# Optimization experiments

Measured on AMD Instinct MI355X. Metric: run time of the kernel, lower is better.

Reference implementation:

```python
import jax, jax.numpy as jnp
import numpy as np

B, N, D, P = 64, 1024, 256, 256


def setup_inputs() -> dict:
    key = jax.random.key(0)
    kx, k1, k2, k4 = jax.random.split(key, 4)
    x = jax.random.normal(kx, (B, N, D), dtype=jnp.float32)
    # weights ~ random_uniform(-0.05, 0.05) in the original; scale here is irrelevant for math
    w1 = jax.random.uniform(k1, (D, P), dtype=jnp.float32, minval=-0.05, maxval=0.05)
    w2 = jax.random.uniform(k2, (D, P), dtype=jnp.float32, minval=-0.05, maxval=0.05)
    w4 = jax.random.uniform(k4, (P, 1), dtype=jnp.float32, minval=-0.05, maxval=0.05)
    return {"x": x, "w1": w1, "w2": w2, "w4": w4}


def reference(x, w1, w2, w4):
    # x: [B, N, D] (already stacked/transposed; query_n=key_n=values=x in the original)
    q = jax.nn.sigmoid(jnp.einsum('bnd,dp->bnp', x, w1))  # [B,N,P]
    k = jax.nn.sigmoid(jnp.einsum('bnd,dp->bnp', x, w2))  # [B,N,P]
    temper = jnp.sqrt(jnp.asarray(w1.shape[1], x.dtype))
    attn = jax.nn.softmax(jnp.einsum('bnp,bmp->bnm', q, k) / temper, axis=2)  # [B,N,N]
    # dropout(0.1) in the original is inference-identity here
    out = jnp.einsum('bnm,bmd->bnd', attn, x)             # [B,N,D]
    a = jax.nn.softmax(jnp.einsum('bnd,do->bno', out, w4), axis=1)  # [B,N,1]
    sentence = jnp.sum(x * a, axis=1)                     # [B,D]
    return sentence
```

## Files before the change

kernel.cpp:

```cpp
#include <hip/hip_runtime.h>
#include <hip/hip_bf16.h>
#include <cstdint>
#include <cstddef>

constexpr int BB = 64;
constexpr int NN = 1024;
constexpr int DD = 256;
constexpr int PP = 256;

typedef short short8 __attribute__((ext_vector_type(8)));
typedef float f32x4 __attribute__((ext_vector_type(4)));

__device__ __forceinline__ unsigned short f2bf(float f) {
    union { __hip_bfloat16 h; unsigned short u; } v;
    v.h = __float2bfloat16(f);
    return v.u;
}

__device__ __forceinline__ void async_load16(void* lds, const void* g) {
    __builtin_amdgcn_global_load_lds(
        (const __attribute__((address_space(1))) unsigned int*)g,
        (__attribute__((address_space(3))) unsigned int*)lds, 16, 0, 0);
}

__device__ __forceinline__ void stage_tile(const unsigned short* src_base,
                                           unsigned short* lds, int wv, int lane) {
    const char* base = (const char*)src_base;
    char* dst0 = (char*)lds + wv * 8192;
    #pragma unroll
    for (int i = 0; i < 8; i++) {
        int row = wv * 16 + i * 2 + (lane >> 5);
        int blk = (lane & 31) ^ (row & 7);
        async_load16(dst0 + i * 1024, base + row * 512 + blk * 16);
    }
}

__device__ __forceinline__ void stage32(const unsigned short* base,
                                        unsigned short* lds, int wv, int lane) {
    char* dst0 = (char*)lds + wv * 4096;
    #pragma unroll
    for (int i = 0; i < 4; i++) {
        int row = wv * 8 + i * 2 + (lane >> 5);
        int blk = (lane & 31) ^ (row & 7);
        async_load16(dst0 + i * 1024, (const char*)base + row * 512 + blk * 16);
    }
}

__device__ __forceinline__ short8 lds_frag(const unsigned short* lds, int row, int kidx) {
    uint32_t byte = (uint32_t)(row * 512) + (uint32_t)(((kidx ^ (row & 7)) & 31) << 4);
    return *reinterpret_cast<const short8*>(reinterpret_cast<const char*>(lds) + byte);
}

__global__ void prep_wt(const float* __restrict__ w1, const float* __restrict__ w2,
                        unsigned short* __restrict__ wt) {
    int j = blockIdx.x;
    int d = threadIdx.x;
    const float* w = (j < PP) ? w1 : w2;
    int jj = j & (PP - 1);
    wt[j * DD + d] = f2bf(w[d * PP + jj]);
}

__global__ __launch_bounds__(256) void qk_fused(const float* __restrict__ x,
                                                const unsigned short* __restrict__ wt,
                                                const float* __restrict__ w4,
                                                unsigned short* __restrict__ qb,
                                                unsigned short* __restrict__ kb,
                                                float* __restrict__ xv) {
    __shared__ __align__(16) unsigned short wtile[2][16384];
    const int t = threadIdx.x, wv = t >> 6, lane = t & 63, l15 = lane & 15, l4 = lane >> 4;
    const int rowBase = blockIdx.x * 128 + wv * 32;

    stage_tile(wt, wtile[0], wv, lane);

    short8 xf[2][8];
    float xvp[2] = {0.f, 0.f};
    #pragma unroll
    for (int kc = 0; kc < 8; kc++) {
        float4 w4a = *reinterpret_cast<const float4*>(w4 + kc * 32 + l4 * 8);
        float4 w4b = *reinterpret_cast<const float4*>(w4 + kc * 32 + l4 * 8 + 4);
        #pragma unroll
        for (int s = 0; s < 2; s++) {
            const float* xr = x + (size_t)(rowBase + s * 16 + l15) * DD + kc * 32 + l4 * 8;
            float4 a = *reinterpret_cast<const float4*>(xr);
            float4 b = *reinterpret_cast<const float4*>(xr + 4);
            xvp[s] += a.x * w4a.x + a.y * w4a.y + a.z * w4a.z + a.w * w4a.w
                    + b.x * w4b.x + b.y * w4b.y + b.z * w4b.z + b.w * w4b.w;
            short8 f;
            f[0] = (short)f2bf(a.x); f[1] = (short)f2bf(a.y);
            f[2] = (short)f2bf(a.z); f[3] = (short)f2bf(a.w);
            f[4] = (short)f2bf(b.x); f[5] = (short)f2bf(b.y);
            f[6] = (short)f2bf(b.z); f[7] = (short)f2bf(b.w);
            xf[s][kc] = f;
        }
    }
    #pragma unroll
    for (int s = 0; s < 2; s++) {
        xvp[s] += __shfl_xor(xvp[s], 16);
        xvp[s] += __shfl_xor(xvp[s], 32);
        if (l4 == 0) xv[rowBase + s * 16 + l15] = xvp[s];
    }

    __syncthreads();
    int buf = 0;
    for (int ct = 0; ct < 8; ct++) {
        if (ct + 1 < 8) stage_tile(wt + (size_t)(ct + 1) * 64 * DD, wtile[buf ^ 1], wv, lane);
        unsigned short* outp = (ct < 4) ? qb : kb;
        const int pc0 = (ct & 3) * 64;
        #pragma unroll
        for (int st = 0; st < 4; st++) {
            f32x4 acc0 = {0.f, 0.f, 0.f, 0.f};
            f32x4 acc1 = {0.f, 0.f, 0.f, 0.f};
            #pragma unroll
            for (int kc = 0; kc < 8; kc++) {
                short8 wf = lds_frag(wtile[buf], st * 16 + l15, kc * 4 + l4);
                acc0 = __builtin_amdgcn_mfma_f32_16x16x32_bf16(wf, xf[0][kc], acc0, 0, 0, 0);
                acc1 = __builtin_amdgcn_mfma_f32_16x16x32_bf16(wf, xf[1][kc], acc1, 0, 0, 0);
            }
            const int pc = pc0 + st * 16 + l4 * 4;
            ushort4 pk;
            pk.x = f2bf(1.f / (1.f + __expf(-acc0[0])));
            pk.y = f2bf(1.f / (1.f + __expf(-acc0[1])));
            pk.z = f2bf(1.f / (1.f + __expf(-acc0[2])));
            pk.w = f2bf(1.f / (1.f + __expf(-acc0[3])));
            *reinterpret_cast<ushort4*>(outp + (size_t)(rowBase + l15) * PP + pc) = pk;
            pk.x = f2bf(1.f / (1.f + __expf(-acc1[0])));
            pk.y = f2bf(1.f / (1.f + __expf(-acc1[1])));
            pk.z = f2bf(1.f / (1.f + __expf(-acc1[2])));
            pk.w = f2bf(1.f / (1.f + __expf(-acc1[3])));
            *reinterpret_cast<ushort4*>(outp + (size_t)(rowBase + 16 + l15) * PP + pc) = pk;
        }
        __syncthreads();
        buf ^= 1;
    }
}

__global__ __launch_bounds__(256, 2) void attn_logit(const unsigned short* __restrict__ qb,
                                                     const unsigned short* __restrict__ kb,
                                                     const float* __restrict__ xv,
                                                     float* __restrict__ numo,
                                                     float* __restrict__ deno) {
    __shared__ __align__(16) unsigned short kt[2][8192];
    __shared__ float xvs[512];
    const int qt = blockIdx.x >> 1, half = blockIdx.x & 1, b = blockIdx.y;
    const int t = threadIdx.x, wv = t >> 6, lane = t & 63, l15 = lane & 15, l4 = lane >> 4;
    const unsigned short* kbb = kb + ((size_t)b * NN + half * 512) * PP;

    stage32(kbb, kt[0], wv, lane);

    xvs[t] = xv[b * NN + half * 512 + t];
    xvs[t + 256] = xv[b * NN + half * 512 + t + 256];

    short8 qf[4][8];
    const int qrow0 = b * NN + qt * 256 + wv * 64;
    #pragma unroll
    for (int s = 0; s < 4; s++) {
        const unsigned short* qrow = qb + (size_t)(qrow0 + s * 16 + l15) * PP;
        #pragma unroll
        for (int kc = 0; kc < 8; kc++)
            qf[s][kc] = *reinterpret_cast<const short8*>(qrow + kc * 32 + l4 * 8);
    }

    float den[4][4], num[4][4];
    #pragma unroll
    for (int s = 0; s < 4; s++)
        #pragma unroll
        for (int r = 0; r < 4; r++) { den[s][r] = 0.f; num[s][r] = 0.f; }

    __syncthreads();
    int buf = 0;
    for (int mc = 0; mc < 16; mc++) {
        if (mc + 1 < 16) stage32(kbb + (size_t)(mc + 1) * 32 * PP, kt[buf ^ 1], wv, lane);
        #pragma unroll
        for (int st = 0; st < 2; st++) {
            f32x4 z = {0.f, 0.f, 0.f, 0.f};
            f32x4 a[4] = {z, z, z, z};
            #pragma unroll
            for (int kc = 0; kc < 8; kc++) {
                short8 kf = lds_frag(kt[buf], st * 16 + l15, kc * 4 + l4);
                a[0] = __builtin_amdgcn_mfma_f32_16x16x32_bf16(qf[0][kc], kf, a[0], 0, 0, 0);
                a[1] = __builtin_amdgcn_mfma_f32_16x16x32_bf16(qf[1][kc], kf, a[1], 0, 0, 0);
                a[2] = __builtin_amdgcn_mfma_f32_16x16x32_bf16(qf[2][kc], kf, a[2], 0, 0, 0);
                a[3] = __builtin_amdgcn_mfma_f32_16x16x32_bf16(qf[3][kc], kf, a[3], 0, 0, 0);
            }
            float xvv = xvs[mc * 32 + st * 16 + l15];
            #pragma unroll
            for (int s = 0; s < 4; s++)
                #pragma unroll
                for (int r = 0; r < 4; r++) {
                    float e = __expf(a[s][r] * 0.0625f);
                    den[s][r] += e;
                    num[s][r] += e * xvv;
                }
        }
        __syncthreads();
        buf ^= 1;
    }
    #pragma unroll
    for (int s = 0; s < 4; s++)
        #pragma unroll
        for (int r = 0; r < 4; r++) {
            #pragma unroll
            for (int off = 1; off < 16; off <<= 1) {
                den[s][r] += __shfl_xor(den[s][r], off);
                num[s][r] += __shfl_xor(num[s][r], off);
            }
        }
    if (l15 == 0) {
        #pragma unroll
        for (int s = 0; s < 4; s++)
            #pragma unroll
            for (int r = 0; r < 4; r++) {
                int n = qt * 256 + wv * 64 + s * 16 + l4 * 4 + r;
                size_t o = (size_t)half * BB * NN + (size_t)b * NN + n;
                numo[o] = num[s][r];
                deno[o] = den[s][r];
            }
    }
}

__global__ __launch_bounds__(256) void sent_partial(const float* __restrict__ x,
                                                    const float* __restrict__ numo,
                                                    const float* __restrict__ deno,
                                                    float* __restrict__ part) {
    __shared__ float al[64];
    __shared__ float redA[4];
    __shared__ float redB[4];
    const int b = blockIdx.x, ch = blockIdx.y;
    const int t = threadIdx.x;
    float l[4];
    #pragma unroll
    for (int i = 0; i < 4; i++) {
        int n = b * NN + t + i * 256;
        l[i] = (numo[n] + numo[BB * NN + n]) / (deno[n] + deno[BB * NN + n]);
    }
    float mx = fmaxf(fmaxf(l[0], l[1]), fmaxf(l[2], l[3]));
    #pragma unroll
    for (int off = 1; off < 64; off <<= 1) mx = fmaxf(mx, __shfl_xor(mx, off));
    if ((t & 63) == 0) redA[t >> 6] = mx;
    __syncthreads();
    mx = fmaxf(fmaxf(redA[0], redA[1]), fmaxf(redA[2], redA[3]));
    float e[4], es = 0.f;
    #pragma unroll
    for (int i = 0; i < 4; i++) { e[i] = __expf(l[i] - mx); es += e[i]; }
    #pragma unroll
    for (int off = 1; off < 64; off <<= 1) es += __shfl_xor(es, off);
    if ((t & 63) == 0) redB[t >> 6] = es;
    __syncthreads();
    float inv = 1.f / (redB[0] + redB[1] + redB[2] + redB[3]);
    int ei = ch >> 2;
    float sel = (ei == 0) ? e[0] : (ei == 1) ? e[1] : (ei == 2) ? e[2] : e[3];
    if ((t >> 6) == (ch & 3)) al[t & 63] = sel * inv;
    __syncthreads();
    float acc = 0.f;
    const float* xb = x + ((size_t)b * NN + ch * 64) * DD + t;
    #pragma unroll 8
    for (int n = 0; n < 64; n++)
        acc += al[n] * xb[(size_t)n * DD];
    part[(b * 16 + ch) * DD + t] = acc;
}

__global__ void sent_final(const float* __restrict__ part, float* __restrict__ out) {
    int b = blockIdx.x, t = threadIdx.x;
    float s = 0.f;
    #pragma unroll
    for (int c = 0; c < 16; c++) s += part[(b * 16 + c) * DD + t];
    out[b * DD + t] = s;
}

extern "C" void kernel_launch(void* const* d_in, const int* in_sizes, int n_in,
                              void* d_out, int out_size, void* d_ws, size_t ws_size,
                              hipStream_t stream) {
    (void)in_sizes; (void)n_in; (void)out_size; (void)ws_size;
    const float* x  = (const float*)d_in[0];
    const float* w1 = (const float*)d_in[1];
    const float* w2 = (const float*)d_in[2];
    const float* w4 = (const float*)d_in[3];
    float* out = (float*)d_out;

    char* ws = (char*)d_ws;
    const size_t MB = 1024 * 1024;
    unsigned short* qb   = (unsigned short*)(ws);
    unsigned short* kb   = (unsigned short*)(ws + 32 * MB);
    unsigned short* wt   = (unsigned short*)(ws + 64 * MB);
    float*          xv   = (float*)(ws + 64 * MB + 256 * 1024);
    float*          num  = (float*)(ws + 64 * MB + 512 * 1024);
    float*          den  = (float*)(ws + 64 * MB + 1024 * 1024);
    float*          part = (float*)(ws);

    prep_wt<<<dim3(2 * PP), dim3(DD), 0, stream>>>(w1, w2, wt);
    qk_fused<<<dim3(BB * NN / 128), dim3(256), 0, stream>>>(x, wt, w4, qb, kb, xv);
    attn_logit<<<dim3(8, BB), dim3(256), 0, stream>>>(qb, kb, xv, num, den);
    sent_partial<<<dim3(BB, 16), dim3(256), 0, stream>>>(x, num, den, part);
    sent_final<<<dim3(BB), dim3(DD), 0, stream>>>(part, out);
}
```

Before: 104.0 us.

## Use single-wave workgroups with triple-buffered async LDS staging and XCD-aware batch mapping

Rewrites qk_fused and attn_logit as 64-thread single-wave workgroups. Each loads 16-row tiles into a 3-deep LDS ring and uses explicit vmcnt waits instead of __syncthreads. attn_logit now covers all 1024 keys per block, so the key-half split and the num/den merge are gone; it writes the final logit directly and maps batches to XCDs for L2 locality. The aim is to remove workgroup barriers and the extra merge traffic, at the cost of more blocks, each re-reading K and W tiles with less sharing across waves.

New measurement: 152.2 us. 46.3% more time.

```diff
diff --git a/kernel.cpp b/kernel.cpp
--- a/kernel.cpp
+++ b/kernel.cpp
@@ -23,26 +23,13 @@
         (__attribute__((address_space(3))) unsigned int*)lds, 16, 0, 0);
 }
 
-__device__ __forceinline__ void stage_tile(const unsigned short* src_base,
-                                           unsigned short* lds, int wv, int lane) {
-    const char* base = (const char*)src_base;
-    char* dst0 = (char*)lds + wv * 8192;
+__device__ __forceinline__ void stage16(const unsigned short* base,
+                                        unsigned short* lds, int lane) {
     #pragma unroll
     for (int i = 0; i < 8; i++) {
-        int row = wv * 16 + i * 2 + (lane >> 5);
+        int row = i * 2 + (lane >> 5);
         int blk = (lane & 31) ^ (row & 7);
-        async_load16(dst0 + i * 1024, base + row * 512 + blk * 16);
-    }
-}
-
-__device__ __forceinline__ void stage32(const unsigned short* base,
-                                        unsigned short* lds, int wv, int lane) {
-    char* dst0 = (char*)lds + wv * 4096;
-    #pragma unroll
-    for (int i = 0; i < 4; i++) {
-        int row = wv * 8 + i * 2 + (lane >> 5);
-        int blk = (lane & 31) ^ (row & 7);
-        async_load16(dst0 + i * 1024, (const char*)base + row * 512 + blk * 16);
+        async_load16((char*)lds + i * 1024, (const char*)base + row * 512 + blk * 16);
     }
 }
 
@@ -60,17 +47,15 @@
     wt[j * DD + d] = f2bf(w[d * PP + jj]);
 }
 
-__global__ __launch_bounds__(256) void qk_fused(const float* __restrict__ x,
-                                                const unsigned short* __restrict__ wt,
-                                                const float* __restrict__ w4,
-                                                unsigned short* __restrict__ qb,
-                                                unsigned short* __restrict__ kb,
-                                                float* __restrict__ xv) {
-    __shared__ __align__(16) unsigned short wtile[2][16384];
-    const int t = threadIdx.x, wv = t >> 6, lane = t & 63, l15 = lane & 15, l4 = lane >> 4;
-    const int rowBase = blockIdx.x * 128 + wv * 32;
-
-    stage_tile(wt, wtile[0], wv, lane);
+__global__ __launch_bounds__(64, 2) void qk_fused(const float* __restrict__ x,
+                                                  const unsigned short* __restrict__ wt,
+                                                  const float* __restrict__ w4,
+                                                  unsigned short* __restrict__ qb,
+                                                  unsigned short* __restrict__ kb,
+                                                  float* __restrict__ xv) {
+    __shared__ __align__(16) unsigned short wtl[3][4096];
+    const int lane = threadIdx.x, l15 = lane & 15, l4 = lane >> 4;
+    const int rowBase = blockIdx.x * 32;
 
     short8 xf[2][8];
     float xvp[2] = {0.f, 0.f};
@@ -100,58 +85,59 @@
         if (l4 == 0) xv[rowBase + s * 16 + l15] = xvp[s];
     }
 
-    __syncthreads();
-    int buf = 0;
-    for (int ct = 0; ct < 8; ct++) {
-        if (ct + 1 < 8) stage_tile(wt + (size_t)(ct + 1) * 64 * DD, wtile[buf ^ 1], wv, lane);
-        unsigned short* outp = (ct < 4) ? qb : kb;
-        const int pc0 = (ct & 3) * 64;
-        #pragma unroll
-        for (int st = 0; st < 4; st++) {
-            f32x4 acc0 = {0.f, 0.f, 0.f, 0.f};
-            f32x4 acc1 = {0.f, 0.f, 0.f, 0.f};
-            #pragma unroll
-            for (int kc = 0; kc < 8; kc++) {
-                short8 wf = lds_frag(wtile[buf], st * 16 + l15, kc * 4 + l4);
-                acc0 = __builtin_amdgcn_mfma_f32_16x16x32_bf16(wf, xf[0][kc], acc0, 0, 0, 0);
-                acc1 = __builtin_amdgcn_mfma_f32_16x16x32_bf16(wf, xf[1][kc], acc1, 0, 0, 0);
-            }
-            const int pc = pc0 + st * 16 + l4 * 4;
-            ushort4 pk;
-            pk.x = f2bf(1.f / (1.f + __expf(-acc0[0])));
-            pk.y = f2bf(1.f / (1.f + __expf(-acc0[1])));
-            pk.z = f2bf(1.f / (1.f + __expf(-acc0[2])));
-            pk.w = f2bf(1.f / (1.f + __expf(-acc0[3])));
-            *reinterpret_cast<ushort4*>(outp + (size_t)(rowBase + l15) * PP + pc) = pk;
-            pk.x = f2bf(1.f / (1.f + __expf(-acc1[0])));
-            pk.y = f2bf(1.f / (1.f + __expf(-acc1[1])));
-            pk.z = f2bf(1.f / (1.f + __expf(-acc1[2])));
-            pk.w = f2bf(1.f / (1.f + __expf(-acc1[3])));
-            *reinterpret_cast<ushort4*>(outp + (size_t)(rowBase + 16 + l15) * PP + pc) = pk;
-        }
-        __syncthreads();
-        buf ^= 1;
-    }
-}
-
-__global__ __launch_bounds__(256, 2) void attn_logit(const unsigned short* __restrict__ qb,
-                                                     const unsigned short* __restrict__ kb,
-                                                     const float* __restrict__ xv,
-                                                     float* __restrict__ numo,
-                                                     float* __restrict__ deno) {
-    __shared__ __align__(16) unsigned short kt[2][8192];
-    __shared__ float xvs[512];
-    const int qt = blockIdx.x >> 1, half = blockIdx.x & 1, b = blockIdx.y;
-    const int t = threadIdx.x, wv = t >> 6, lane = t & 63, l15 = lane & 15, l4 = lane >> 4;
-    const unsigned short* kbb = kb + ((size_t)b * NN + half * 512) * PP;
-
-    stage32(kbb, kt[0], wv, lane);
-
-    xvs[t] = xv[b * NN + half * 512 + t];
-    xvs[t + 256] = xv[b * NN + half * 512 + t + 256];
+    stage16(wt, wtl[0], lane);
+    stage16(wt + 16 * DD, wtl[1], lane);
+
+    for (int ct = 0; ct < 32; ct++) {
+        const unsigned short* cur = wtl[ct % 3];
+        if (ct + 2 < 32) {
+            stage16(wt + (size_t)(ct + 2) * 16 * DD, wtl[(ct + 2) % 3], lane);
+            asm volatile("s_waitcnt vmcnt(16)" ::: "memory");
+        } else if (ct + 1 < 32) {
+            asm volatile("s_waitcnt vmcnt(8)" ::: "memory");
+        } else {
+            asm volatile("s_waitcnt vmcnt(0)" ::: "memory");
+        }
+        __builtin_amdgcn_sched_barrier(0);
+        f32x4 acc0 = {0.f, 0.f, 0.f, 0.f};
+        f32x4 acc1 = {0.f, 0.f, 0.f, 0.f};
+        #pragma unroll
+        for (int kc = 0; kc < 8; kc++) {
+            short8 wf = lds_frag(cur, l15, kc * 4 + l4);
+            acc0 = __builtin_amdgcn_mfma_f32_16x16x32_bf16(wf, xf[0][kc], acc0, 0, 0, 0);
+            acc1 = __builtin_amdgcn_mfma_f32_16x16x32_bf16(wf, xf[1][kc], acc1, 0, 0, 0);
+        }
+        unsigned short* outp = (ct < 16) ? qb : kb;
+        const int pc = (ct & 15) * 16 + l4 * 4;
+        ushort4 pk;
+        pk.x = f2bf(1.f / (1.f + __expf(-acc0[0])));
+        pk.y = f2bf(1.f / (1.f + __expf(-acc0[1])));
+        pk.z = f2bf(1.f / (1.f + __expf(-acc0[2])));
+        pk.w = f2bf(1.f / (1.f + __expf(-acc0[3])));
+        *reinterpret_cast<ushort4*>(outp + (size_t)(rowBase + l15) * PP + pc) = pk;
+        pk.x = f2bf(1.f / (1.f + __expf(-acc1[0])));
+        pk.y = f2bf(1.f / (1.f + __expf(-acc1[1])));
+        pk.z = f2bf(1.f / (1.f + __expf(-acc1[2])));
+        pk.w = f2bf(1.f / (1.f + __expf(-acc1[3])));
+        *reinterpret_cast<ushort4*>(outp + (size_t)(rowBase + 16 + l15) * PP + pc) = pk;
+    }
+}
+
+__global__ __launch_bounds__(64, 2) void attn_logit(const unsigned short* __restrict__ qb,
+                                                    const unsigned short* __restrict__ kb,
+                                                    const float* __restrict__ xv,
+                                                    float* __restrict__ lgt) {
+    __shared__ __align__(16) unsigned short kt[3][4096];
+    __shared__ __align__(16) float xvs[1024];
+    const int lane = threadIdx.x, l15 = lane & 15, l4 = lane >> 4;
+    const int wg = blockIdx.x;
+    const int xcd = wg & 7, rest = wg >> 3;
+    const int qt = rest & 15;
+    const int b = (rest >> 4) * 8 + xcd;
+    const unsigned short* kbb = kb + (size_t)b * NN * PP;
 
     short8 qf[4][8];
-    const int qrow0 = b * NN + qt * 256 + wv * 64;
+    const int qrow0 = b * NN + qt * 64;
     #pragma unroll
     for (int s = 0; s < 4; s++) {
         const unsigned short* qrow = qb + (size_t)(qrow0 + s * 16 + l15) * PP;
@@ -160,40 +146,48 @@
             qf[s][kc] = *reinterpret_cast<const short8*>(qrow + kc * 32 + l4 * 8);
     }
 
+    #pragma unroll
+    for (int i = 0; i < 4; i++)
+        async_load16((char*)xvs + i * 1024, (const char*)(xv + b * NN + i * 256) + lane * 16);
+    stage16(kbb, kt[0], lane);
+    stage16(kbb + 16 * PP, kt[1], lane);
+
     float den[4][4], num[4][4];
     #pragma unroll
     for (int s = 0; s < 4; s++)
         #pragma unroll
         for (int r = 0; r < 4; r++) { den[s][r] = 0.f; num[s][r] = 0.f; }
 
-    __syncthreads();
-    int buf = 0;
-    for (int mc = 0; mc < 16; mc++) {
-        if (mc + 1 < 16) stage32(kbb + (size_t)(mc + 1) * 32 * PP, kt[buf ^ 1], wv, lane);
-        #pragma unroll
-        for (int st = 0; st < 2; st++) {
-            f32x4 z = {0.f, 0.f, 0.f, 0.f};
-            f32x4 a[4] = {z, z, z, z};
+    for (int mc = 0; mc < 64; mc++) {
+        const unsigned short* cur = kt[mc % 3];
+        if (mc + 2 < 64) {
+            stage16(kbb + (size_t)(mc + 2) * 16 * PP, kt[(mc + 2) % 3], lane);
+            asm volatile("s_waitcnt vmcnt(16)" ::: "memory");
+        } else if (mc + 1 < 64) {
+            asm volatile("s_waitcnt vmcnt(8)" ::: "memory");
+        } else {
+            asm volatile("s_waitcnt vmcnt(0)" ::: "memory");
+        }
+        __builtin_amdgcn_sched_barrier(0);
+        f32x4 z = {0.f, 0.f, 0.f, 0.f};
+        f32x4 a[4] = {z, z, z, z};
+        #pragma unroll
+        for (int kc = 0; kc < 8; kc++) {
+            short8 kf = lds_frag(cur, l15, kc * 4 + l4);
+            a[0] = __builtin_amdgcn_mfma_f32_16x16x32_bf16(qf[0][kc], kf, a[0], 0, 0, 0);
+            a[1] = __builtin_amdgcn_mfma_f32_16x16x32_bf16(qf[1][kc], kf, a[1], 0, 0, 0);
+            a[2] = __builtin_amdgcn_mfma_f32_16x16x32_bf16(qf[2][kc], kf, a[2], 0, 0, 0);
+            a[3] = __builtin_amdgcn_mfma_f32_16x16x32_bf16(qf[3][kc], kf, a[3], 0, 0, 0);
+        }
+        float xvv = xvs[mc * 16 + l15];
+        #pragma unroll
+        for (int s = 0; s < 4; s++)
             #pragma unroll
-            for (int kc = 0; kc < 8; kc++) {
-                short8 kf = lds_frag(kt[buf], st * 16 + l15, kc * 4 + l4);
-                a[0] = __builtin_amdgcn_mfma_f32_16x16x32_bf16(qf[0][kc], kf, a[0], 0, 0, 0);
-                a[1] = __builtin_amdgcn_mfma_f32_16x16x32_bf16(qf[1][kc], kf, a[1], 0, 0, 0);
-                a[2] = __builtin_amdgcn_mfma_f32_16x16x32_bf16(qf[2][kc], kf, a[2], 0, 0, 0);
-                a[3] = __builtin_amdgcn_mfma_f32_16x16x32_bf16(qf[3][kc], kf, a[3], 0, 0, 0);
+            for (int r = 0; r < 4; r++) {
+                float e = __expf(a[s][r] * 0.0625f);
+                den[s][r] += e;
+                num[s][r] += e * xvv;
             }
-            float xvv = xvs[mc * 32 + st * 16 + l15];
-            #pragma unroll
-            for (int s = 0; s < 4; s++)
-                #pragma unroll
-                for (int r = 0; r < 4; r++) {
-                    float e = __expf(a[s][r] * 0.0625f);
-                    den[s][r] += e;
-                    num[s][r] += e * xvv;
-                }
-        }
-        __syncthreads();
-        buf ^= 1;
     }
     #pragma unroll
     for (int s = 0; s < 4; s++)
@@ -207,20 +201,19 @@
         }
     if (l15 == 0) {
         #pragma unroll
-        for (int s = 0; s < 4; s++)
-            #pragma unroll
-            for (int r = 0; r < 4; r++) {
-                int n = qt * 256 + wv * 64 + s * 16 + l4 * 4 + r;
-                size_t o = (size_t)half * BB * NN + (size_t)b * NN + n;
-                numo[o] = num[s][r];
-                deno[o] = den[s][r];
-            }
+        for (int s = 0; s < 4; s++) {
+            float4 o;
+            o.x = num[s][0] / den[s][0];
+            o.y = num[s][1] / den[s][1];
+            o.z = num[s][2] / den[s][2];
+            o.w = num[s][3] / den[s][3];
+            *reinterpret_cast<float4*>(lgt + b * NN + qt * 64 + s * 16 + l4 * 4) = o;
+        }
     }
 }
 
 __global__ __launch_bounds__(256) void sent_partial(const float* __restrict__ x,
-                                                    const float* __restrict__ numo,
-                                                    const float* __restrict__ deno,
+                                                    const float* __restrict__ lgt,
                                                     float* __restrict__ part) {
     __shared__ float al[64];
     __shared__ float redA[4];
@@ -229,10 +222,7 @@
     const int t = threadIdx.x;
     float l[4];
     #pragma unroll
-    for (int i = 0; i < 4; i++) {
-        int n = b * NN + t + i * 256;
-        l[i] = (numo[n] + numo[BB * NN + n]) / (deno[n] + deno[BB * NN + n]);
-    }
+    for (int i = 0; i < 4; i++) l[i] = lgt[b * NN + t + i * 256];
     float mx = fmaxf(fmaxf(l[0], l[1]), fmaxf(l[2], l[3]));
     #pragma unroll
     for (int off = 1; off < 64; off <<= 1) mx = fmaxf(mx, __shfl_xor(mx, off));
@@ -283,13 +273,12 @@
     unsigned short* kb   = (unsigned short*)(ws + 32 * MB);
     unsigned short* wt   = (unsigned short*)(ws + 64 * MB);
     float*          xv   = (float*)(ws + 64 * MB + 256 * 1024);
-    float*          num  = (float*)(ws + 64 * MB + 512 * 1024);
-    float*          den  = (float*)(ws + 64 * MB + 1024 * 1024);
+    float*          lgt  = (float*)(ws + 64 * MB + 512 * 1024);
     float*          part = (float*)(ws);
 
     prep_wt<<<dim3(2 * PP), dim3(DD), 0, stream>>>(w1, w2, wt);
-    qk_fused<<<dim3(BB * NN / 128), dim3(256), 0, stream>>>(x, wt, w4, qb, kb, xv);
-    attn_logit<<<dim3(8, BB), dim3(256), 0, stream>>>(qb, kb, xv, num, den);
-    sent_partial<<<dim3(BB, 16), dim3(256), 0, stream>>>(x, num, den, part);
+    qk_fused<<<dim3(BB * NN / 32), dim3(64), 0, stream>>>(x, wt, w4, qb, kb, xv);
+    attn_logit<<<dim3(BB * 16), dim3(64), 0, stream>>>(qb, kb, xv, lgt);
+    sent_partial<<<dim3(BB, 16), dim3(256), 0, stream>>>(x, lgt, part);
     sent_final<<<dim3(BB), dim3(DD), 0, stream>>>(part, out);
 }
```

## Restructure QK projection and logit kernels to keep x and K tiles resident in LDS

Applied to the files above, without the earlier changes.

qk_fused now stages a bf16 copy of the 128-row x tile in LDS once and has each of 8 waves hold its weight fragments in registers, instead of double-buffering weight tiles through LDS. attn_logit now loads a full 256-row K quarter into 128KB of LDS once and loops over all 1024 queries in two passes, removing per-chunk staging and barriers. Partial num/den results are split four ways and summed in sent_partial. The larger LDS footprint and 512-thread blocks may limit occupancy, and the q fragments are read from global memory four times.

Result: slower. 113.7 us (+9.4%).

```diff
diff --git a/kernel.cpp b/kernel.cpp
--- a/kernel.cpp
+++ b/kernel.cpp
@@ -21,29 +21,6 @@
     __builtin_amdgcn_global_load_lds(
         (const __attribute__((address_space(1))) unsigned int*)g,
         (__attribute__((address_space(3))) unsigned int*)lds, 16, 0, 0);
-}
-
-__device__ __forceinline__ void stage_tile(const unsigned short* src_base,
-                                           unsigned short* lds, int wv, int lane) {
-    const char* base = (const char*)src_base;
-    char* dst0 = (char*)lds + wv * 8192;
-    #pragma unroll
-    for (int i = 0; i < 8; i++) {
-        int row = wv * 16 + i * 2 + (lane >> 5);
-        int blk = (lane & 31) ^ (row & 7);
-        async_load16(dst0 + i * 1024, base + row * 512 + blk * 16);
-    }
-}
-
-__device__ __forceinline__ void stage32(const unsigned short* base,
-                                        unsigned short* lds, int wv, int lane) {
-    char* dst0 = (char*)lds + wv * 4096;
-    #pragma unroll
-    for (int i = 0; i < 4; i++) {
-        int row = wv * 8 + i * 2 + (lane >> 5);
-        int blk = (lane & 31) ^ (row & 7);
-        async_load16(dst0 + i * 1024, (const char*)base + row * 512 + blk * 16);
-    }
 }
 
 __device__ __forceinline__ short8 lds_frag(const unsigned short* lds, int row, int kidx) {
@@ -60,129 +37,130 @@
     wt[j * DD + d] = f2bf(w[d * PP + jj]);
 }
 
-__global__ __launch_bounds__(256) void qk_fused(const float* __restrict__ x,
-                                                const unsigned short* __restrict__ wt,
-                                                const float* __restrict__ w4,
-                                                unsigned short* __restrict__ qb,
-                                                unsigned short* __restrict__ kb,
-                                                float* __restrict__ xv) {
-    __shared__ __align__(16) unsigned short wtile[2][16384];
+__global__ __launch_bounds__(512, 4) void qk_fused(const float* __restrict__ x,
+                                                   const unsigned short* __restrict__ wt,
+                                                   const float* __restrict__ w4,
+                                                   unsigned short* __restrict__ qb,
+                                                   unsigned short* __restrict__ kb,
+                                                   float* __restrict__ xv) {
+    __shared__ __align__(16) unsigned short xs[128 * 256];
     const int t = threadIdx.x, wv = t >> 6, lane = t & 63, l15 = lane & 15, l4 = lane >> 4;
-    const int rowBase = blockIdx.x * 128 + wv * 32;
-
-    stage_tile(wt, wtile[0], wv, lane);
-
-    short8 xf[2][8];
-    float xvp[2] = {0.f, 0.f};
-    #pragma unroll
-    for (int kc = 0; kc < 8; kc++) {
-        float4 w4a = *reinterpret_cast<const float4*>(w4 + kc * 32 + l4 * 8);
-        float4 w4b = *reinterpret_cast<const float4*>(w4 + kc * 32 + l4 * 8 + 4);
-        #pragma unroll
-        for (int s = 0; s < 2; s++) {
-            const float* xr = x + (size_t)(rowBase + s * 16 + l15) * DD + kc * 32 + l4 * 8;
-            float4 a = *reinterpret_cast<const float4*>(xr);
-            float4 b = *reinterpret_cast<const float4*>(xr + 4);
-            xvp[s] += a.x * w4a.x + a.y * w4a.y + a.z * w4a.z + a.w * w4a.w
-                    + b.x * w4b.x + b.y * w4b.y + b.z * w4b.z + b.w * w4b.w;
+    const int xbase = blockIdx.x * 128;
+
+    {
+        const int row = t >> 2, cb = t & 3;
+        const float* xr = x + (size_t)(xbase + row) * DD + cb * 64;
+        const float* w4r = w4 + cb * 64;
+        float xvp = 0.f;
+        #pragma unroll
+        for (int j = 0; j < 8; j++) {
+            float4 a = *reinterpret_cast<const float4*>(xr + j * 8);
+            float4 bq = *reinterpret_cast<const float4*>(xr + j * 8 + 4);
+            float4 wa = *reinterpret_cast<const float4*>(w4r + j * 8);
+            float4 wb = *reinterpret_cast<const float4*>(w4r + j * 8 + 4);
+            xvp += a.x * wa.x + a.y * wa.y + a.z * wa.z + a.w * wa.w
+                 + bq.x * wb.x + bq.y * wb.y + bq.z * wb.z + bq.w * wb.w;
             short8 f;
-            f[0] = (short)f2bf(a.x); f[1] = (short)f2bf(a.y);
-            f[2] = (short)f2bf(a.z); f[3] = (short)f2bf(a.w);
-            f[4] = (short)f2bf(b.x); f[5] = (short)f2bf(b.y);
-            f[6] = (short)f2bf(b.z); f[7] = (short)f2bf(b.w);
-            xf[s][kc] = f;
-        }
-    }
-    #pragma unroll
-    for (int s = 0; s < 2; s++) {
-        xvp[s] += __shfl_xor(xvp[s], 16);
-        xvp[s] += __shfl_xor(xvp[s], 32);
-        if (l4 == 0) xv[rowBase + s * 16 + l15] = xvp[s];
-    }
-
-    __syncthreads();
-    int buf = 0;
-    for (int ct = 0; ct < 8; ct++) {
-        if (ct + 1 < 8) stage_tile(wt + (size_t)(ct + 1) * 64 * DD, wtile[buf ^ 1], wv, lane);
-        unsigned short* outp = (ct < 4) ? qb : kb;
-        const int pc0 = (ct & 3) * 64;
-        #pragma unroll
-        for (int st = 0; st < 4; st++) {
+            f[0] = (short)f2bf(a.x);  f[1] = (short)f2bf(a.y);
+            f[2] = (short)f2bf(a.z);  f[3] = (short)f2bf(a.w);
+            f[4] = (short)f2bf(bq.x); f[5] = (short)f2bf(bq.y);
+            f[6] = (short)f2bf(bq.z); f[7] = (short)f2bf(bq.w);
+            int blk = cb * 8 + j;
+            uint32_t byte = (uint32_t)(row * 512) + (uint32_t)((blk ^ (row & 7)) << 4);
+            *reinterpret_cast<short8*>(reinterpret_cast<char*>(xs) + byte) = f;
+        }
+        xvp += __shfl_xor(xvp, 1);
+        xvp += __shfl_xor(xvp, 2);
+        if (cb == 0) xv[xbase + row] = xvp;
+    }
+    __syncthreads();
+
+    for (int h = 0; h < 2; h++) {
+        short8 wf[2][8];
+        #pragma unroll
+        for (int pt = 0; pt < 2; pt++)
+            #pragma unroll
+            for (int kc = 0; kc < 8; kc++)
+                wf[pt][kc] = *reinterpret_cast<const short8*>(
+                    wt + (size_t)(h * 256 + wv * 32 + pt * 16 + l15) * DD + kc * 32 + l4 * 8);
+        unsigned short* outp = h ? kb : qb;
+        for (int set = 0; set < 8; set++) {
             f32x4 acc0 = {0.f, 0.f, 0.f, 0.f};
             f32x4 acc1 = {0.f, 0.f, 0.f, 0.f};
             #pragma unroll
             for (int kc = 0; kc < 8; kc++) {
-                short8 wf = lds_frag(wtile[buf], st * 16 + l15, kc * 4 + l4);
-                acc0 = __builtin_amdgcn_mfma_f32_16x16x32_bf16(wf, xf[0][kc], acc0, 0, 0, 0);
-                acc1 = __builtin_amdgcn_mfma_f32_16x16x32_bf16(wf, xf[1][kc], acc1, 0, 0, 0);
+                short8 af = lds_frag(xs, set * 16 + l15, kc * 4 + l4);
+                acc0 = __builtin_amdgcn_mfma_f32_16x16x32_bf16(wf[0][kc], af, acc0, 0, 0, 0);
+                acc1 = __builtin_amdgcn_mfma_f32_16x16x32_bf16(wf[1][kc], af, acc1, 0, 0, 0);
             }
-            const int pc = pc0 + st * 16 + l4 * 4;
             ushort4 pk;
+            size_t rowoff = (size_t)(xbase + set * 16 + l15) * PP + wv * 32;
             pk.x = f2bf(1.f / (1.f + __expf(-acc0[0])));
             pk.y = f2bf(1.f / (1.f + __expf(-acc0[1])));
             pk.z = f2bf(1.f / (1.f + __expf(-acc0[2])));
             pk.w = f2bf(1.f / (1.f + __expf(-acc0[3])));
-            *reinterpret_cast<ushort4*>(outp + (size_t)(rowBase + l15) * PP + pc) = pk;
+            *reinterpret_cast<ushort4*>(outp + rowoff + l4 * 4) = pk;
             pk.x = f2bf(1.f / (1.f + __expf(-acc1[0])));
             pk.y = f2bf(1.f / (1.f + __expf(-acc1[1])));
             pk.z = f2bf(1.f / (1.f + __expf(-acc1[2])));
             pk.w = f2bf(1.f / (1.f + __expf(-acc1[3])));
-            *reinterpret_cast<ushort4*>(outp + (size_t)(rowBase + 16 + l15) * PP + pc) = pk;
-        }
-        __syncthreads();
-        buf ^= 1;
-    }
-}
-
-__global__ __launch_bounds__(256, 2) void attn_logit(const unsigned short* __restrict__ qb,
+            *reinterpret_cast<ushort4*>(outp + rowoff + 16 + l4 * 4) = pk;
+        }
+    }
+}
+
+__global__ __launch_bounds__(512, 2) void attn_logit(const unsigned short* __restrict__ qb,
                                                      const unsigned short* __restrict__ kb,
                                                      const float* __restrict__ xv,
                                                      float* __restrict__ numo,
                                                      float* __restrict__ deno) {
-    __shared__ __align__(16) unsigned short kt[2][8192];
-    __shared__ float xvs[512];
-    const int qt = blockIdx.x >> 1, half = blockIdx.x & 1, b = blockIdx.y;
+    __shared__ __align__(16) unsigned short kq[256 * 256];
+    __shared__ float xvs[256];
     const int t = threadIdx.x, wv = t >> 6, lane = t & 63, l15 = lane & 15, l4 = lane >> 4;
-    const unsigned short* kbb = kb + ((size_t)b * NN + half * 512) * PP;
-
-    stage32(kbb, kt[0], wv, lane);
-
-    xvs[t] = xv[b * NN + half * 512 + t];
-    xvs[t + 256] = xv[b * NN + half * 512 + t + 256];
-
-    short8 qf[4][8];
-    const int qrow0 = b * NN + qt * 256 + wv * 64;
-    #pragma unroll
-    for (int s = 0; s < 4; s++) {
-        const unsigned short* qrow = qb + (size_t)(qrow0 + s * 16 + l15) * PP;
-        #pragma unroll
-        for (int kc = 0; kc < 8; kc++)
-            qf[s][kc] = *reinterpret_cast<const short8*>(qrow + kc * 32 + l4 * 8);
-    }
-
-    float den[4][4], num[4][4];
-    #pragma unroll
-    for (int s = 0; s < 4; s++)
-        #pragma unroll
-        for (int r = 0; r < 4; r++) { den[s][r] = 0.f; num[s][r] = 0.f; }
-
-    __syncthreads();
-    int buf = 0;
-    for (int mc = 0; mc < 16; mc++) {
-        if (mc + 1 < 16) stage32(kbb + (size_t)(mc + 1) * 32 * PP, kt[buf ^ 1], wv, lane);
-        #pragma unroll
-        for (int st = 0; st < 2; st++) {
+    const int quarter = blockIdx.x, b = blockIdx.y;
+    const unsigned short* kbb = kb + ((size_t)b * NN + quarter * 256) * PP;
+
+    {
+        char* dst0 = (char*)kq + wv * 16384;
+        #pragma unroll
+        for (int i = 0; i < 16; i++) {
+            int row = wv * 32 + i * 2 + (lane >> 5);
+            int blk = (lane & 31) ^ (row & 7);
+            async_load16(dst0 + i * 1024, (const char*)kbb + row * 512 + blk * 16);
+        }
+    }
+    if (t < 256) xvs[t] = xv[b * NN + quarter * 256 + t];
+    __syncthreads();
+
+    #pragma unroll 1
+    for (int p = 0; p < 2; p++) {
+        short8 qf[4][8];
+        const int q0 = b * NN + p * 512 + wv * 64;
+        #pragma unroll
+        for (int s = 0; s < 4; s++) {
+            const unsigned short* qrow = qb + (size_t)(q0 + s * 16 + l15) * PP;
+            #pragma unroll
+            for (int kc = 0; kc < 8; kc++)
+                qf[s][kc] = *reinterpret_cast<const short8*>(qrow + kc * 32 + l4 * 8);
+        }
+        float den[4][4], num[4][4];
+        #pragma unroll
+        for (int s = 0; s < 4; s++)
+            #pragma unroll
+            for (int r = 0; r < 4; r++) { den[s][r] = 0.f; num[s][r] = 0.f; }
+
+        for (int mc = 0; mc < 16; mc++) {
             f32x4 z = {0.f, 0.f, 0.f, 0.f};
             f32x4 a[4] = {z, z, z, z};
             #pragma unroll
             for (int kc = 0; kc < 8; kc++) {
-                short8 kf = lds_frag(kt[buf], st * 16 + l15, kc * 4 + l4);
+                short8 kf = lds_frag(kq, mc * 16 + l15, kc * 4 + l4);
                 a[0] = __builtin_amdgcn_mfma_f32_16x16x32_bf16(qf[0][kc], kf, a[0], 0, 0, 0);
                 a[1] = __builtin_amdgcn_mfma_f32_16x16x32_bf16(qf[1][kc], kf, a[1], 0, 0, 0);
                 a[2] = __builtin_amdgcn_mfma_f32_16x16x32_bf16(qf[2][kc], kf, a[2], 0, 0, 0);
                 a[3] = __builtin_amdgcn_mfma_f32_16x16x32_bf16(qf[3][kc], kf, a[3], 0, 0, 0);
             }
-            float xvv = xvs[mc * 32 + st * 16 + l15];
+            float xvv = xvs[mc * 16 + l15];
             #pragma unroll
             for (int s = 0; s < 4; s++)
                 #pragma unroll
@@ -192,29 +170,27 @@
                     num[s][r] += e * xvv;
                 }
         }
-        __syncthreads();
-        buf ^= 1;
-    }
-    #pragma unroll
-    for (int s = 0; s < 4; s++)
-        #pragma unroll
-        for (int r = 0; r < 4; r++) {
-            #pragma unroll
-            for (int off = 1; off < 16; off <<= 1) {
-                den[s][r] += __shfl_xor(den[s][r], off);
-                num[s][r] += __shfl_xor(num[s][r], off);
+        #pragma unroll
+        for (int s = 0; s < 4; s++)
+            #pragma unroll
+            for (int r = 0; r < 4; r++) {
+                #pragma unroll
+                for (int off = 1; off < 16; off <<= 1) {
+                    den[s][r] += __shfl_xor(den[s][r], off);
+                    num[s][r] += __shfl_xor(num[s][r], off);
+                }
             }
-        }
-    if (l15 == 0) {
-        #pragma unroll
-        for (int s = 0; s < 4; s++)
-            #pragma unroll
-            for (int r = 0; r < 4; r++) {
-                int n = qt * 256 + wv * 64 + s * 16 + l4 * 4 + r;
-                size_t o = (size_t)half * BB * NN + (size_t)b * NN + n;
-                numo[o] = num[s][r];
-                deno[o] = den[s][r];
-            }
+        if (l15 == 0) {
+            #pragma unroll
+            for (int s = 0; s < 4; s++)
+                #pragma unroll
+                for (int r = 0; r < 4; r++) {
+                    int n = p * 512 + wv * 64 + s * 16 + l4 * 4 + r;
+                    size_t o = (size_t)quarter * BB * NN + (size_t)b * NN + n;
+                    numo[o] = num[s][r];
+                    deno[o] = den[s][r];
+                }
+        }
     }
 }
 
@@ -231,7 +207,13 @@
     #pragma unroll
     for (int i = 0; i < 4; i++) {
         int n = b * NN + t + i * 256;
-        l[i] = (numo[n] + numo[BB * NN + n]) / (deno[n] + deno[BB * NN + n]);
+        float ns = 0.f, ds = 0.f;
+        #pragma unroll
+        for (int q = 0; q < 4; q++) {
+            ns += numo[(size_t)q * BB * NN + n];
+            ds += deno[(size_t)q * BB * NN + n];
+        }
+        l[i] = ns / ds;
     }
     float mx = fmaxf(fmaxf(l[0], l[1]), fmaxf(l[2], l[3]));
     #pragma unroll
@@ -284,12 +266,12 @@
     unsigned short* wt   = (unsigned short*)(ws + 64 * MB);
     float*          xv   = (float*)(ws + 64 * MB + 256 * 1024);
     float*          num  = (float*)(ws + 64 * MB + 512 * 1024);
-    float*          den  = (float*)(ws + 64 * MB + 1024 * 1024);
+    float*          den  = (float*)(ws + 64 * MB + 1536 * 1024);
     float*          part = (float*)(ws);
 
     prep_wt<<<dim3(2 * PP), dim3(DD), 0, stream>>>(w1, w2, wt);
-    qk_fused<<<dim3(BB * NN / 128), dim3(256), 0, stream>>>(x, wt, w4, qb, kb, xv);
-    attn_logit<<<dim3(8, BB), dim3(256), 0, stream>>>(qb, kb, xv, num, den);
+    qk_fused<<<dim3(BB * NN / 128), dim3(512), 0, stream>>>(x, wt, w4, qb, kb, xv);
+    attn_logit<<<dim3(4, BB), dim3(512), 0, stream>>>(qb, kb, xv, num, den);
     sent_partial<<<dim3(BB, 16), dim3(256), 0, stream>>>(x, num, den, part);
     sent_final<<<dim3(BB), dim3(DD), 0, stream>>>(part, out);
 }
```
